# Kernel tuning notes

Measured on AMD Instinct MI355X. Metric: run time of the kernel, lower is better.

Reference implementation:

```python
import jax, jax.numpy as jnp
import numpy as np

B, S, E, H = 4, 2048, 1024, 16
D = E // H  # head_dim = 64


def setup_inputs() -> dict:
    key = jax.random.key(0)
    ks = jax.random.split(key, 9)
    scale = 1.0 / np.sqrt(E)
    return {
        "x": jax.random.normal(ks[0], (B, S, E), dtype=jnp.float32),
        "Wq": jax.random.normal(ks[1], (E, E), dtype=jnp.float32) * scale,
        "bq": jax.random.normal(ks[2], (E,), dtype=jnp.float32) * 0.01,
        "Wk": jax.random.normal(ks[3], (E, E), dtype=jnp.float32) * scale,
        "bk": jax.random.normal(ks[4], (E,), dtype=jnp.float32) * 0.01,
        "Wv": jax.random.normal(ks[5], (E, E), dtype=jnp.float32) * scale,
        "bv": jax.random.normal(ks[6], (E,), dtype=jnp.float32) * 0.01,
        "Wo": jax.random.normal(ks[7], (E, E), dtype=jnp.float32) * scale,
        "bo": jax.random.normal(ks[8], (E,), dtype=jnp.float32) * 0.01,
    }


def reference(x, Wq, bq, Wk, bk, Wv, bv, Wo, bo):
    b, s, e = x.shape
    # Linear projections (torch Linear: y = x @ W.T + b), split into heads: [b, h, s, d]
    def proj(W, bias):
        return (x @ W.T + bias).reshape(b, s, H, D).transpose(0, 2, 1, 3)

    q = proj(Wq, bq)
    k = proj(Wk, bk)
    v = proj(Wv, bv)

    # scores: [b, h, s, s], scaled by 1/sqrt(head_dim)
    scores = jnp.einsum("bhqd,bhkd->bhqk", q, k) / jnp.sqrt(jnp.float32(D))
    probs = jax.nn.softmax(scores, axis=-1)
    # dropout_rate=0.0 -> identity

    # weighted values: [b, h, s, d] -> [b, s, e]
    out = jnp.einsum("bhqk,bhkd->bhqd", probs, v)
    out = out.transpose(0, 2, 1, 3).reshape(b, s, e)
    return out @ Wo.T + bo
```

## Files before the change

### kernel.cpp

```cpp
#include <hip/hip_runtime.h>
#include <hip/hip_bf16.h>
#include <math.h>

#define B_ 4
#define S_ 2048
#define E_ 1024
#define H_ 16
#define D_ 64
#define MTOT (B_ * S_)

typedef __attribute__((ext_vector_type(8))) short short8;
typedef __attribute__((ext_vector_type(4))) float f32x4;
typedef __attribute__((ext_vector_type(16))) float f32x16;
typedef unsigned short u16;
typedef unsigned int u32;

static __device__ __forceinline__ u16 bfbits(float x) {
  __hip_bfloat16 h = __float2bfloat16(x);
  return *reinterpret_cast<u16*>(&h);
}
static __device__ __forceinline__ u32 pk2(float a, float b) {
  return (u32)bfbits(a) | ((u32)bfbits(b) << 16);
}

static __device__ __forceinline__ void gload_lds16(const void* g, void* l) {
  __builtin_amdgcn_global_load_lds(
      (const __attribute__((address_space(1))) u32*)g,
      (__attribute__((address_space(3))) u32*)l, 16, 0, 0);
}

static __device__ __forceinline__ void plane_swap(u32& a, u32& b) {
#if __has_builtin(__builtin_amdgcn_permlane32_swap)
  auto r = __builtin_amdgcn_permlane32_swap(a, b, false, false);
  a = r[0];
  b = r[1];
#else
  const u32 as = __shfl_xor(a, 32);
  const u32 bs = __shfl_xor(b, 32);
  const int hi = (threadIdx.x & 63) >> 5;
  const u32 na = hi ? bs : a;
  const u32 nb = hi ? b : as;
  a = na;
  b = nb;
#endif
}

static __device__ __forceinline__ void cvtseg(const float* __restrict__ in,
                                              u16* __restrict__ out, int n4,
                                              int tid, int stride) {
  for (int i = tid; i < n4; i += stride) {
    const float4 v = reinterpret_cast<const float4*>(in)[i];
    ushort4 o;
    o.x = bfbits(v.x); o.y = bfbits(v.y); o.z = bfbits(v.z); o.w = bfbits(v.w);
    reinterpret_cast<ushort4*>(out)[i] = o;
  }
}

__global__ __launch_bounds__(256) void f2bf5(
    const float* __restrict__ x, const float* __restrict__ w0,
    const float* __restrict__ w1, const float* __restrict__ w2,
    const float* __restrict__ w3, u16* __restrict__ xo, u16* __restrict__ o0,
    u16* __restrict__ o1, u16* __restrict__ o2, u16* __restrict__ o3, int nx4,
    int nw4) {
  const int tid = blockIdx.x * blockDim.x + threadIdx.x;
  const int stride = gridDim.x * blockDim.x;
  cvtseg(x, xo, nx4, tid, stride);
  cvtseg(w0, o0, nw4, tid, stride);
  cvtseg(w1, o1, nw4, tid, stride);
  cvtseg(w2, o2, nw4, tid, stride);
  cvtseg(w3, o3, nw4, tid, stride);
}

__global__ __launch_bounds__(256) void gemm_qkv(
    const u16* __restrict__ xb, const u16* __restrict__ wq,
    const u16* __restrict__ wk, const u16* __restrict__ wv,
    const float* __restrict__ bq, const float* __restrict__ bk,
    const float* __restrict__ bv, u16* __restrict__ qo, u16* __restrict__ ko,
    u16* __restrict__ vto, float qscale) {
  __shared__ u16 As[128 * 32];
  __shared__ u16 Bs[128 * 32];

  const int bid = blockIdx.x;
  const int wg = ((bid & 7) * 192) + (bid >> 3);
  const int bx = wg % 24, by = wg / 24;

  const int tid = threadIdx.x;
  const int lane = tid & 63;
  const int w = tid >> 6;
  const int wr = w >> 1, wc = w & 1;
  const int m0 = by << 7;
  const int seg = bx >> 3;
  const int ncol0 = (bx & 7) << 7;
  const int l15 = lane & 15, l4 = lane >> 4;

  const u16* Bsel = seg == 0 ? wq : (seg == 1 ? wk : wv);
  const float* biasSel = seg == 0 ? bq : (seg == 1 ? bk : bv);

  f32x4 acc[4][4];
#pragma unroll
  for (int i = 0; i < 4; ++i)
#pragma unroll
    for (int j = 0; j < 4; ++j) {
      f32x4 z = {0.f, 0.f, 0.f, 0.f};
      acc[i][j] = z;
    }

  const int srow = w << 5;
  const u16* Ag =
      xb + (size_t)(m0 + srow + (lane >> 2)) * E_ + ((lane & 3) << 3);
  const u16* Bg =
      Bsel + (size_t)(ncol0 + srow + (lane >> 2)) * E_ + ((lane & 3) << 3);
  u16* AsW = As + srow * 32;
  u16* BsW = Bs + srow * 32;
  const size_t rstep = (size_t)16 * E_;

  const u16* Afrag = As + ((wr << 6) + l15) * 32 + (l4 << 3);
  const u16* Bfrag = Bs + ((wc << 6) + l15) * 32 + (l4 << 3);

  for (int k0 = 0; k0 < E_; k0 += 32) {
    gload_lds16(Ag + k0, AsW);
    gload_lds16(Ag + rstep + k0, AsW + 512);
    gload_lds16(Bg + k0, BsW);
    gload_lds16(Bg + rstep + k0, BsW + 512);
    __syncthreads();
    short8 a[4], b[4];
#pragma unroll
    for (int i = 0; i < 4; ++i) a[i] = *(const short8*)(Afrag + i * 512);
#pragma unroll
    for (int j = 0; j < 4; ++j) b[j] = *(const short8*)(Bfrag + j * 512);
#pragma unroll
    for (int i = 0; i < 4; ++i)
#pragma unroll
      for (int j = 0; j < 4; ++j)
        acc[i][j] = __builtin_amdgcn_mfma_f32_16x16x32_bf16(a[i], b[j],
                                                            acc[i][j], 0, 0, 0);
    __syncthreads();
  }

  const int mbase = m0 + (wr << 6);
  const int nbase = ncol0 + (wc << 6);

  if (seg < 2) {
    u16* out = seg ? ko : qo;
    const float al = seg ? 1.f : qscale;
#pragma unroll
    for (int ni = 0; ni < 4; ++ni) {
      const int n = nbase + ni * 16 + l15;
      const int hh = n >> 6, d = n & 63;
      const float bn = biasSel[n];
#pragma unroll
      for (int mi = 0; mi < 4; ++mi)
#pragma unroll
        for (int r = 0; r < 4; ++r) {
          const int m = mbase + mi * 16 + (l4 << 2) + r;
          const int bb = m >> 11, s = m & (S_ - 1);
          out[(((size_t)(bb * H_ + hh) * S_ + s) << 6) + d] =
              bfbits((acc[mi][ni][r] + bn) * al);
        }
    }
  } else {
#pragma unroll
    for (int ni = 0; ni < 4; ++ni) {
      const int n = nbase + ni * 16 + l15;
      const float bn = biasSel[n];
#pragma unroll
      for (int mi = 0; mi < 4; ++mi) {
        const int m = mbase + mi * 16 + (l4 << 2);
        ushort4 pk;
        pk.x = bfbits(acc[mi][ni][0] + bn);
        pk.y = bfbits(acc[mi][ni][1] + bn);
        pk.z = bfbits(acc[mi][ni][2] + bn);
        pk.w = bfbits(acc[mi][ni][3] + bn);
        *(ushort4*)(vto + (size_t)n * MTOT + m) = pk;
      }
    }
  }
}

__global__ __launch_bounds__(256) void gemm_out(
    const u16* __restrict__ A, const u16* __restrict__ Bw,
    const float* __restrict__ bias, float* __restrict__ out, int M, int N,
    int K) {
  __shared__ u16 As[128 * 32];
  __shared__ u16 Bs[128 * 32];

  const int tid = threadIdx.x;
  const int lane = tid & 63;
  const int w = tid >> 6;
  const int wr = w >> 1, wc = w & 1;
  const int m0 = blockIdx.y << 7, n0 = blockIdx.x << 7;
  const int l15 = lane & 15, l4 = lane >> 4;

  f32x4 acc[4][4];
#pragma unroll
  for (int i = 0; i < 4; ++i)
#pragma unroll
    for (int j = 0; j < 4; ++j) {
      f32x4 z = {0.f, 0.f, 0.f, 0.f};
      acc[i][j] = z;
    }

  const int srow = w << 5;
  const u16* Ag = A + (size_t)(m0 + srow + (lane >> 2)) * K + ((lane & 3) << 3);
  const u16* Bg = Bw + (size_t)(n0 + srow + (lane >> 2)) * K + ((lane & 3) << 3);
  u16* AsW = As + srow * 32;
  u16* BsW = Bs + srow * 32;
  const size_t rstep = (size_t)16 * K;

  const u16* Afrag = As + ((wr << 6) + l15) * 32 + (l4 << 3);
  const u16* Bfrag = Bs + ((wc << 6) + l15) * 32 + (l4 << 3);

  for (int k0 = 0; k0 < K; k0 += 32) {
    gload_lds16(Ag + k0, AsW);
    gload_lds16(Ag + rstep + k0, AsW + 512);
    gload_lds16(Bg + k0, BsW);
    gload_lds16(Bg + rstep + k0, BsW + 512);
    __syncthreads();
    short8 a[4], b[4];
#pragma unroll
    for (int i = 0; i < 4; ++i) a[i] = *(const short8*)(Afrag + i * 512);
#pragma unroll
    for (int j = 0; j < 4; ++j) b[j] = *(const short8*)(Bfrag + j * 512);
#pragma unroll
    for (int i = 0; i < 4; ++i)
#pragma unroll
      for (int j = 0; j < 4; ++j)
        acc[i][j] = __builtin_amdgcn_mfma_f32_16x16x32_bf16(a[i], b[j],
                                                            acc[i][j], 0, 0, 0);
    __syncthreads();
  }

  const int mbase = m0 + (wr << 6);
  const int nbase = n0 + (wc << 6);
#pragma unroll
  for (int ni = 0; ni < 4; ++ni) {
    const int n = nbase + ni * 16 + l15;
    const float bn = bias[n];
#pragma unroll
    for (int mi = 0; mi < 4; ++mi)
#pragma unroll
      for (int r = 0; r < 4; ++r) {
        const int m = mbase + mi * 16 + (l4 << 2) + r;
        out[(size_t)m * N + n] = acc[mi][ni][r] + bn;
      }
  }
}

__global__ __launch_bounds__(256) void attn_mfma4(
    const u16* __restrict__ Q, const u16* __restrict__ K,
    const u16* __restrict__ Vt, u16* __restrict__ out) {
  __shared__ u16 pool[16384];
  u16* Ksb = pool;
  u16* Vsb = pool + 8192;

  const int tid = threadIdx.x;
  const int lane = tid & 63;
  const int w = tid >> 6;
  const int l31 = lane & 31, hi = lane >> 5;
  const int bh = blockIdx.y;
  const int b = bh >> 4, h = bh & 15;
  const int q0 = blockIdx.x << 7;
  const int qw = q0 + (w << 5);

  const u16* Qg = Q + ((size_t)bh * S_ + qw + l31) * D_ + (hi << 3);
  short8 qf[4];
#pragma unroll
  for (int ks = 0; ks < 4; ++ks) qf[ks] = *(const short8*)(Qg + (ks << 4));

  f32x16 o0, o1, fz;
#pragma unroll
  for (int u = 0; u < 16; ++u) { o0[u] = 0.f; o1[u] = 0.f; fz[u] = 0.f; }
  float l_r = 0.f;

  const int rr = lane >> 3;
  const int cs = (lane & 7) ^ rr;
  const u16* Kg = K + ((size_t)bh * S_ + (w << 4) + rr) * D_ + (cs << 3);
  const u16* Vg = Vt + ((size_t)((h << 6) + (w << 4) + rr)) * MTOT +
                  (size_t)b * S_ + (cs << 3);

#define STAGE(bufi, kt)                                   \
  do {                                                    \
    u16* kd = Ksb + (bufi)*4096 + (w << 10);              \
    u16* vd = Vsb + (bufi)*4096 + (w << 10);              \
    gload_lds16(Kg + (size_t)(kt)*D_, kd);                \
    gload_lds16(Kg + (size_t)((kt) + 8) * D_, kd + 512);  \
    gload_lds16(Vg + (kt), vd);                           \
    gload_lds16(Vg + (size_t)8 * MTOT + (kt), vd + 512);  \
  } while (0)

  STAGE(0, 0);
  __syncthreads();

  for (int t = 0; t < S_ / 64; ++t) {
    const int cur = t & 1;
    if (t + 1 < S_ / 64) STAGE(cur ^ 1, (t + 1) << 6);

    const u16* KsB = Ksb + cur * 4096;
    const u16* VsB = Vsb + cur * 4096;

    f32x16 s0, s1;
    __builtin_amdgcn_s_setprio(1);
    {
      const int ch = (hi ^ (l31 & 7)) << 3;
      const short8 k0 = *(const short8*)&KsB[(l31 << 6) + ch];
      const short8 k1 = *(const short8*)&KsB[((32 + l31) << 6) + ch];
      s0 = __builtin_amdgcn_mfma_f32_32x32x16_bf16(k0, qf[0], fz, 0, 0, 0);
      s1 = __builtin_amdgcn_mfma_f32_32x32x16_bf16(k1, qf[0], fz, 0, 0, 0);
    }
#pragma unroll
    for (int ks = 1; ks < 4; ++ks) {
      const int ch = (((ks << 1) + hi) ^ (l31 & 7)) << 3;
      const short8 k0 = *(const short8*)&KsB[(l31 << 6) + ch];
      const short8 k1 = *(const short8*)&KsB[((32 + l31) << 6) + ch];
      s0 = __builtin_amdgcn_mfma_f32_32x32x16_bf16(k0, qf[ks], s0, 0, 0, 0);
      s1 = __builtin_amdgcn_mfma_f32_32x32x16_bf16(k1, qf[ks], s1, 0, 0, 0);
    }
    __builtin_amdgcn_s_setprio(0);

#pragma unroll
    for (int u = 0; u < 16; ++u) {
      s0[u] = exp2f(s0[u] - 16.f);
      s1[u] = exp2f(s1[u] - 16.f);
    }
    float a16[16];
#pragma unroll
    for (int u = 0; u < 16; ++u) a16[u] = s0[u] + s1[u];
#pragma unroll
    for (int st = 8; st > 0; st >>= 1)
#pragma unroll
      for (int u = 0; u < 16; ++u)
        if (u < st) a16[u] += a16[u + st];
    l_r += a16[0];

    short8 pf[4];
#pragma unroll
    for (int ks2 = 0; ks2 < 4; ++ks2) {
      const int ub = (ks2 << 3) & 15;
#define EV(u) (((ks2 << 3) + (u)) < 16 ? s0 : s1)[(ub + (u)) & 15]
      u32 a0 = pk2(EV(0), EV(1));
      u32 a0b = pk2(EV(2), EV(3));
      u32 a1 = pk2(EV(4), EV(5));
      u32 a1b = pk2(EV(6), EV(7));
#undef EV
      plane_swap(a0, a1);
      plane_swap(a0b, a1b);
      union { u32 wd[4]; short8 v; } pu;
      pu.wd[0] = a0; pu.wd[1] = a0b; pu.wd[2] = a1; pu.wd[3] = a1b;
      pf[ks2] = pu.v;
    }

    __builtin_amdgcn_s_setprio(1);
#pragma unroll
    for (int ks2 = 0; ks2 < 4; ++ks2) {
      const int ch = (((ks2 << 1) + hi) ^ (l31 & 7)) << 3;
      const short8 v0 = *(const short8*)&VsB[(l31 << 6) + ch];
      const short8 v1 = *(const short8*)&VsB[((32 + l31) << 6) + ch];
      o0 = __builtin_amdgcn_mfma_f32_32x32x16_bf16(v0, pf[ks2], o0, 0, 0, 0);
      o1 = __builtin_amdgcn_mfma_f32_32x32x16_bf16(v1, pf[ks2], o1, 0, 0, 0);
    }
    __builtin_amdgcn_s_setprio(0);
    __syncthreads();
  }

  const float inv = 1.f / (l_r + __shfl_xor(l_r, 32));
  u16* ep = pool + w * 2304;
  const int g = l31 >> 3;
#pragma unroll
  for (int t2 = 0; t2 < 2; ++t2) {
#pragma unroll
    for (int reg = 0; reg < 16; reg += 2) {
      const int d = (t2 << 5) + ((reg >> 2) << 3) + (hi << 2) + (reg & 3);
      const int ds = (((d >> 3) ^ g) << 3) | (d & 7);
      const float x0 = (t2 ? o1[reg] : o0[reg]) * inv;
      const float x1 = (t2 ? o1[reg + 1] : o0[reg + 1]) * inv;
      *(u32*)&ep[l31 * 72 + ds] = pk2(x0, x1);
    }
  }
  __builtin_amdgcn_s_waitcnt(0);
#pragma unroll
  for (int pass = 0; pass < 4; ++pass) {
    const int row = (pass << 3) + (lane >> 3);
    const int cc = lane & 7;
    const short8 t8 = *(const short8*)&ep[row * 72 + ((cc ^ pass) << 3)];
    *(short8*)(out + ((size_t)(b * S_ + q0 + (w << 5) + row)) * E_ + (h << 6) +
               (cc << 3)) = t8;
  }
}

extern "C" void kernel_launch(void* const* d_in, const int* in_sizes, int n_in,
                              void* d_out, int out_size, void* d_ws,
                              size_t ws_size, hipStream_t stream) {
  const float* x  = (const float*)d_in[0];
  const float* Wq = (const float*)d_in[1];
  const float* bq = (const float*)d_in[2];
  const float* Wk = (const float*)d_in[3];
  const float* bk = (const float*)d_in[4];
  const float* Wv = (const float*)d_in[5];
  const float* bv = (const float*)d_in[6];
  const float* Wo = (const float*)d_in[7];
  const float* bo = (const float*)d_in[8];

  u16* wsp = (u16*)d_ws;
  const size_t nx = (size_t)MTOT * E_;
  const size_t nw = (size_t)E_ * E_;
  u16* xb  = wsp;
  u16* wqb = xb + nx;
  u16* wkb = wqb + nw;
  u16* wvb = wkb + nw;
  u16* wob = wvb + nw;
  u16* qb  = wob + nw;
  u16* kb  = qb + nx;
  u16* vtb = kb + nx;
  u16* ab  = vtb + nx;

  const dim3 blk(256);
  const float qscale = 0.125f * 1.4426950408889634f;

  hipLaunchKernelGGL(f2bf5, dim3(2048), blk, 0, stream, x, Wq, Wk, Wv, Wo, xb,
                     wqb, wkb, wvb, wob, (int)(nx / 4), (int)(nw / 4));
  hipLaunchKernelGGL(gemm_qkv, dim3(1536), blk, 0, stream, xb, wqb, wkb, wvb,
                     bq, bk, bv, qb, kb, vtb, qscale);
  hipLaunchKernelGGL(attn_mfma4, dim3(S_ / 128, B_ * H_), blk, 0, stream, qb,
                     kb, vtb, ab);
  hipLaunchKernelGGL(gemm_out, dim3(E_ / 128, MTOT / 128), blk, 0, stream, ab,
                     wob, bo, (float*)d_out, MTOT, E_, E_);
}
```

Measured before the change: 337.9 us.

## Double-buffer LDS in projection GEMMs, swizzle out-GEMM blocks, flatten conversion

Both projection GEMMs now use two LDS buffers so the global-to-LDS load of the next K tile is issued before computing the current one, which removes one barrier per iteration and overlaps load latency with MFMA work. The output GEMM switches to a 1D grid with an XCD-aware block remap, like the QKV GEMM, and hardcodes its dimensions. The fp32-to-bf16 conversion becomes a single flat grid-stride loop over all five tensors. LDS use per block doubles, which can lower occupancy. Only one barrier now guards each buffer swap, so correctness relies on the trailing barrier in the loop.

```diff
diff --git a/kernel.cpp b/kernel.cpp
--- a/kernel.cpp
+++ b/kernel.cpp
@@ -45,30 +45,34 @@
 #endif
 }
 
-static __device__ __forceinline__ void cvtseg(const float* __restrict__ in,
-                                              u16* __restrict__ out, int n4,
-                                              int tid, int stride) {
-  for (int i = tid; i < n4; i += stride) {
-    const float4 v = reinterpret_cast<const float4*>(in)[i];
-    ushort4 o;
-    o.x = bfbits(v.x); o.y = bfbits(v.y); o.z = bfbits(v.z); o.w = bfbits(v.w);
-    reinterpret_cast<ushort4*>(out)[i] = o;
-  }
-}
-
-__global__ __launch_bounds__(256) void f2bf5(
+__global__ __launch_bounds__(256) void f2bf_flat(
     const float* __restrict__ x, const float* __restrict__ w0,
     const float* __restrict__ w1, const float* __restrict__ w2,
     const float* __restrict__ w3, u16* __restrict__ xo, u16* __restrict__ o0,
-    u16* __restrict__ o1, u16* __restrict__ o2, u16* __restrict__ o3, int nx4,
-    int nw4) {
-  const int tid = blockIdx.x * blockDim.x + threadIdx.x;
-  const int stride = gridDim.x * blockDim.x;
-  cvtseg(x, xo, nx4, tid, stride);
-  cvtseg(w0, o0, nw4, tid, stride);
-  cvtseg(w1, o1, nw4, tid, stride);
-  cvtseg(w2, o2, nw4, tid, stride);
-  cvtseg(w3, o3, nw4, tid, stride);
+    u16* __restrict__ o1, u16* __restrict__ o2, u16* __restrict__ o3) {
+  const int nx4 = (MTOT * E_) / 4;
+  const int nw4 = (E_ * E_) / 4;
+  const int tot = nx4 + 4 * nw4;
+  int i = blockIdx.x * 256 + threadIdx.x;
+  const int stride = gridDim.x * 256;
+  for (; i < tot; i += stride) {
+    const float* src;
+    u16* dst;
+    int off;
+    if (i < nx4) {
+      src = x; dst = xo; off = i;
+    } else {
+      const int j = i - nx4;
+      const int seg = j >> 18;
+      off = j & (nw4 - 1);
+      src = seg == 0 ? w0 : seg == 1 ? w1 : seg == 2 ? w2 : w3;
+      dst = seg == 0 ? o0 : seg == 1 ? o1 : seg == 2 ? o2 : o3;
+    }
+    const float4 v = reinterpret_cast<const float4*>(src)[off];
+    ushort4 o;
+    o.x = bfbits(v.x); o.y = bfbits(v.y); o.z = bfbits(v.z); o.w = bfbits(v.w);
+    reinterpret_cast<ushort4*>(dst)[off] = o;
+  }
 }
 
 __global__ __launch_bounds__(256) void gemm_qkv(
@@ -77,8 +81,8 @@
     const float* __restrict__ bq, const float* __restrict__ bk,
     const float* __restrict__ bv, u16* __restrict__ qo, u16* __restrict__ ko,
     u16* __restrict__ vto, float qscale) {
-  __shared__ u16 As[128 * 32];
-  __shared__ u16 Bs[128 * 32];
+  __shared__ u16 As[2][128 * 32];
+  __shared__ u16 Bs[2][128 * 32];
 
   const int bid = blockIdx.x;
   const int wg = ((bid & 7) * 192) + (bid >> 3);
@@ -110,19 +114,26 @@
       xb + (size_t)(m0 + srow + (lane >> 2)) * E_ + ((lane & 3) << 3);
   const u16* Bg =
       Bsel + (size_t)(ncol0 + srow + (lane >> 2)) * E_ + ((lane & 3) << 3);
-  u16* AsW = As + srow * 32;
-  u16* BsW = Bs + srow * 32;
   const size_t rstep = (size_t)16 * E_;
 
-  const u16* Afrag = As + ((wr << 6) + l15) * 32 + (l4 << 3);
-  const u16* Bfrag = Bs + ((wc << 6) + l15) * 32 + (l4 << 3);
+#define QSTAGE(bufi, k0)                                  \
+  do {                                                    \
+    u16* ad = As[bufi] + srow * 32;                       \
+    u16* bd = Bs[bufi] + srow * 32;                       \
+    gload_lds16(Ag + (k0), ad);                           \
+    gload_lds16(Ag + rstep + (k0), ad + 512);             \
+    gload_lds16(Bg + (k0), bd);                           \
+    gload_lds16(Bg + rstep + (k0), bd + 512);             \
+  } while (0)
+
+  QSTAGE(0, 0);
+  __syncthreads();
+  int cur = 0;
 
   for (int k0 = 0; k0 < E_; k0 += 32) {
-    gload_lds16(Ag + k0, AsW);
-    gload_lds16(Ag + rstep + k0, AsW + 512);
-    gload_lds16(Bg + k0, BsW);
-    gload_lds16(Bg + rstep + k0, BsW + 512);
-    __syncthreads();
+    if (k0 + 32 < E_) QSTAGE(cur ^ 1, k0 + 32);
+    const u16* Afrag = As[cur] + ((wr << 6) + l15) * 32 + (l4 << 3);
+    const u16* Bfrag = Bs[cur] + ((wc << 6) + l15) * 32 + (l4 << 3);
     short8 a[4], b[4];
 #pragma unroll
     for (int i = 0; i < 4; ++i) a[i] = *(const short8*)(Afrag + i * 512);
@@ -135,6 +146,7 @@
         acc[i][j] = __builtin_amdgcn_mfma_f32_16x16x32_bf16(a[i], b[j],
                                                             acc[i][j], 0, 0, 0);
     __syncthreads();
+    cur ^= 1;
   }
 
   const int mbase = m0 + (wr << 6);
@@ -179,16 +191,18 @@
 
 __global__ __launch_bounds__(256) void gemm_out(
     const u16* __restrict__ A, const u16* __restrict__ Bw,
-    const float* __restrict__ bias, float* __restrict__ out, int M, int N,
-    int K) {
-  __shared__ u16 As[128 * 32];
-  __shared__ u16 Bs[128 * 32];
+    const float* __restrict__ bias, float* __restrict__ out) {
+  __shared__ u16 As[2][128 * 32];
+  __shared__ u16 Bs[2][128 * 32];
+
+  const int bid = blockIdx.x;
+  const int wg = ((bid & 7) * 64) + (bid >> 3);
+  const int n0 = (wg & 7) << 7, m0 = (wg >> 3) << 7;
 
   const int tid = threadIdx.x;
   const int lane = tid & 63;
   const int w = tid >> 6;
   const int wr = w >> 1, wc = w & 1;
-  const int m0 = blockIdx.y << 7, n0 = blockIdx.x << 7;
   const int l15 = lane & 15, l4 = lane >> 4;
 
   f32x4 acc[4][4];
@@ -201,21 +215,18 @@
     }
 
   const int srow = w << 5;
-  const u16* Ag = A + (size_t)(m0 + srow + (lane >> 2)) * K + ((lane & 3) << 3);
-  const u16* Bg = Bw + (size_t)(n0 + srow + (lane >> 2)) * K + ((lane & 3) << 3);
-  u16* AsW = As + srow * 32;
-  u16* BsW = Bs + srow * 32;
-  const size_t rstep = (size_t)16 * K;
-
-  const u16* Afrag = As + ((wr << 6) + l15) * 32 + (l4 << 3);
-  const u16* Bfrag = Bs + ((wc << 6) + l15) * 32 + (l4 << 3);
-
-  for (int k0 = 0; k0 < K; k0 += 32) {
-    gload_lds16(Ag + k0, AsW);
-    gload_lds16(Ag + rstep + k0, AsW + 512);
-    gload_lds16(Bg + k0, BsW);
-    gload_lds16(Bg + rstep + k0, BsW + 512);
-    __syncthreads();
+  const u16* Ag = A + (size_t)(m0 + srow + (lane >> 2)) * E_ + ((lane & 3) << 3);
+  const u16* Bg = Bw + (size_t)(n0 + srow + (lane >> 2)) * E_ + ((lane & 3) << 3);
+  const size_t rstep = (size_t)16 * E_;
+
+  QSTAGE(0, 0);
+  __syncthreads();
+  int cur = 0;
+
+  for (int k0 = 0; k0 < E_; k0 += 32) {
+    if (k0 + 32 < E_) QSTAGE(cur ^ 1, k0 + 32);
+    const u16* Afrag = As[cur] + ((wr << 6) + l15) * 32 + (l4 << 3);
+    const u16* Bfrag = Bs[cur] + ((wc << 6) + l15) * 32 + (l4 << 3);
     short8 a[4], b[4];
 #pragma unroll
     for (int i = 0; i < 4; ++i) a[i] = *(const short8*)(Afrag + i * 512);
@@ -228,6 +239,7 @@
         acc[i][j] = __builtin_amdgcn_mfma_f32_16x16x32_bf16(a[i], b[j],
                                                             acc[i][j], 0, 0, 0);
     __syncthreads();
+    cur ^= 1;
   }
 
   const int mbase = m0 + (wr << 6);
@@ -241,7 +253,7 @@
 #pragma unroll
       for (int r = 0; r < 4; ++r) {
         const int m = mbase + mi * 16 + (l4 << 2) + r;
-        out[(size_t)m * N + n] = acc[mi][ni][r] + bn;
+        out[(size_t)m * E_ + n] = acc[mi][ni][r] + bn;
       }
   }
 }
@@ -416,12 +428,12 @@
   const dim3 blk(256);
   const float qscale = 0.125f * 1.4426950408889634f;
 
-  hipLaunchKernelGGL(f2bf5, dim3(2048), blk, 0, stream, x, Wq, Wk, Wv, Wo, xb,
-                     wqb, wkb, wvb, wob, (int)(nx / 4), (int)(nw / 4));
+  hipLaunchKernelGGL(f2bf_flat, dim3(2048), blk, 0, stream, x, Wq, Wk, Wv, Wo,
+                     xb, wqb, wkb, wvb, wob);
   hipLaunchKernelGGL(gemm_qkv, dim3(1536), blk, 0, stream, xb, wqb, wkb, wvb,
                      bq, bk, bv, qb, kb, vtb, qscale);
   hipLaunchKernelGGL(attn_mfma4, dim3(S_ / 128, B_ * H_), blk, 0, stream, qb,
                      kb, vtb, ab);
-  hipLaunchKernelGGL(gemm_out, dim3(E_ / 128, MTOT / 128), blk, 0, stream, ab,
-                     wob, bo, (float*)d_out, MTOT, E_, E_);
-}
+  hipLaunchKernelGGL(gemm_out, dim3(512), blk, 0, stream, ab, wob, bo,
+                     (float*)d_out);
+}
```

Result: no change. 340.5 us (+0.8%).
